# Kernel optimization log

Measured on AMD Instinct MI355X. Metric: run time of the kernel, lower is better.

## Reference

```python
import jax, jax.numpy as jnp
import numpy as np

N_FM = 100000; N_TP = 4096; N_SM = 100000
IN_FM = 64; IN_SM = 32; IN_TP = 32; IN_GF = 64; HID = 128
E_QOQ = 1000000; E_BP = 1000000; E_CP = 500000; E_CD = 500000; E_RB = 1000000


def setup_inputs():
    key = jax.random.key(0)
    ks = jax.random.split(key, 32)
    rn = lambda k, s, sc=0.05: jax.random.normal(k, s, jnp.float32) * sc
    inp = {}
    inp['x_fm'] = jax.random.normal(ks[0], (N_FM, IN_FM), jnp.float32)
    inp['x_sm'] = jax.random.normal(ks[1], (N_SM, IN_SM), jnp.float32)
    inp['period_vol'] = jax.random.uniform(ks[2], (N_TP, 1), jnp.float32)
    inp['gf'] = jax.random.normal(ks[3], (1, IN_GF), jnp.float32)
    inp['pe_table'] = rn(ks[4], (N_TP, IN_TP), 1.0)  # period_emb weight
    inp['qoq_src'] = jax.random.randint(ks[5], (E_QOQ,), 0, N_FM)
    inp['qoq_dst'] = jax.random.randint(ks[6], (E_QOQ,), 0, N_FM)
    inp['bp_src'] = jax.random.randint(ks[7], (E_BP,), 0, N_FM)
    inp['bp_dst'] = jax.random.randint(ks[8], (E_BP,), 0, N_TP)
    inp['cp_src'] = jax.random.randint(ks[9], (E_CP,), 0, N_TP)
    inp['cp_dst'] = jax.random.randint(ks[10], (E_CP,), 0, N_FM)
    inp['cd_src'] = jax.random.randint(ks[11], (E_CD,), 0, N_TP)
    inp['cd_dst'] = jax.random.randint(ks[12], (E_CD,), 0, N_SM)
    inp['rb_src'] = jax.random.randint(ks[13], (E_RB,), 0, N_TP)
    inp['rb_dst'] = jax.random.randint(ks[14], (E_RB,), 0, N_FM)
    i = 15
    # per-relation SAGEConv params: W_l [in_src,H] + bias, W_r [in_dst,H] (root, no bias)
    for name, ins, ind in [('qoq', IN_FM, IN_FM), ('bp', IN_FM, IN_TP), ('cp', IN_TP, IN_FM), ('cd', IN_TP, IN_SM), ('rb', IN_TP, IN_FM)]:
        inp[name + '_Wl'] = rn(ks[i], (ins, HID)); inp[name + '_bl'] = jnp.zeros((HID,), jnp.float32)
        inp[name + '_Wr'] = rn(ks[i + 1], (ind, HID)); i += 2
    for t in ['fm', 'tp', 'sm']:
        inp['ln_' + t + '_g'] = jnp.ones((HID,), jnp.float32)
        inp['ln_' + t + '_b'] = jnp.zeros((HID,), jnp.float32)
    inp['head_W1'] = rn(ks[i], (HID * 3 + IN_GF, HID // 2)); inp['head_b1'] = jnp.zeros((HID // 2,), jnp.float32)
    inp['head_W2'] = rn(ks[i + 1], (HID // 2, 1)); inp['head_b2'] = jnp.zeros((1,), jnp.float32)
    return inp


def _seg_mean(feat, dst, n):
    s = jax.ops.segment_sum(feat, dst, num_segments=n)
    c = jax.ops.segment_sum(jnp.ones((dst.shape[0], 1), feat.dtype), dst, num_segments=n)
    return s / jnp.maximum(c, 1.0)


def _sage(x_src, x_dst, src, dst, Wl, bl, Wr):
    # PyG SAGEConv: lin_l(mean_j x_j) + lin_r(x_i); aggregate raw features, then transform
    m = _seg_mean(x_src[src], dst, x_dst.shape[0])
    return m @ Wl + bl + x_dst @ Wr


def _ln(x, g, b, eps=1e-5):
    mu = x.mean(-1, keepdims=True)
    xc = x - mu
    var = (xc * xc).mean(-1, keepdims=True)
    return xc / jnp.sqrt(var + eps) * g + b


def _forward(x_fm, x_sm, period_vol, gf, pe_table,
             qoq_Wl, qoq_bl, qoq_Wr, bp_Wl, bp_bl, bp_Wr, cp_Wl, cp_bl, cp_Wr,
             cd_Wl, cd_bl, cd_Wr, rb_Wl, rb_bl, rb_Wr,
             ln_fm_g, ln_fm_b, ln_tp_g, ln_tp_b, ln_sm_g, ln_sm_b,
             head_W1, head_b1, head_W2, head_b2,
             qoq_src, qoq_dst, bp_src, bp_dst, cp_src, cp_dst, cd_src, cd_dst, rb_src, rb_dst):
    pe = pe_table * period_vol  # [T, in_tp]
    # HeteroConv aggr='mean': average relation outputs per destination type
    out_fm = (_sage(x_fm, x_fm, qoq_src, qoq_dst, qoq_Wl, qoq_bl, qoq_Wr)
              + _sage(pe, x_fm, cp_src, cp_dst, cp_Wl, cp_bl, cp_Wr)
              + _sage(pe, x_fm, rb_src, rb_dst, rb_Wl, rb_bl, rb_Wr)) / 3.0
    out_tp = _sage(x_fm, pe, bp_src, bp_dst, bp_Wl, bp_bl, bp_Wr)
    out_sm = _sage(pe, x_sm, cd_src, cd_dst, cd_Wl, cd_bl, cd_Wr)
    fm = jax.nn.relu(_ln(out_fm, ln_fm_g, ln_fm_b))
    tp = jax.nn.relu(_ln(out_tp, ln_tp_g, ln_tp_b))
    sm = jax.nn.relu(_ln(out_sm, ln_sm_g, ln_sm_b))
    h = jnp.concatenate([fm.mean(0), tp.mean(0), sm.mean(0), gf[0]], axis=-1)
    h = jax.nn.relu(h @ head_W1 + head_b1)  # dropout is identity in eval
    return (h @ head_W2 + head_b2).squeeze()


def reference(x_fm, x_sm, period_vol, gf, pe_table,
              qoq_src, qoq_dst, bp_src, bp_dst, cp_src, cp_dst, cd_src, cd_dst, rb_src, rb_dst,
              qoq_Wl, qoq_bl, qoq_Wr, bp_Wl, bp_bl, bp_Wr, cp_Wl, cp_bl, cp_Wr,
              cd_Wl, cd_bl, cd_Wr, rb_Wl, rb_bl, rb_Wr,
              ln_fm_g, ln_fm_b, ln_tp_g, ln_tp_b, ln_sm_g, ln_sm_b,
              head_W1, head_b1, head_W2, head_b2):
    return _forward(x_fm, x_sm, period_vol, gf, pe_table,
                    qoq_Wl, qoq_bl, qoq_Wr, bp_Wl, bp_bl, bp_Wr, cp_Wl, cp_bl, cp_Wr,
                    cd_Wl, cd_bl, cd_Wr, rb_Wl, rb_bl, rb_Wr,
                    ln_fm_g, ln_fm_b, ln_tp_g, ln_tp_b, ln_sm_g, ln_sm_b,
                    head_W1, head_b1, head_W2, head_b2,
                    qoq_src, qoq_dst, bp_src, bp_dst, cp_src, cp_dst, cd_src, cd_dst, rb_src, rb_dst)
```

## Files before the change

### kernel.cpp

```cpp
#include <hip/hip_runtime.h>
#include <hip/hip_fp16.h>

#define N_FM 100000
#define N_TP 4096
#define N_SM 100000
#define HID 128
#define E_QOQ 1000000
#define E_BP 1000000
#define E_CP 500000
#define E_CD 500000
#define E_RB 1000000
#define E_TOT 4000000

#define EO_CP  1000000
#define EO_RB  1500000
#define EO_BP  2500000
#define EO_CD  3500000

#define EL_QOQ 0
#define EL_CP  (N_FM)
#define EL_RB  (2 * N_FM)
#define EL_BP  (3 * N_FM)
#define EL_CD  (3 * N_FM + N_TP)
#define NTOT   (3 * N_FM + N_TP + N_SM)

#define BB_QOQ 0
#define BB_CP  782
#define BB_RB  1173
#define BB_BP  1564
#define BB_CD  1692
#define NBUCK  2083
#define CHUNK  4096
#define NCHUNK ((E_TOT + CHUNK - 1) / CHUNK)
#define EPB    (CHUNK / 256)

#define PAIRS_CAP 5784064

#define GRID_FM 768
#define GRID_TP 64
#define GRID_SM 1024

__device__ __forceinline__ int bucket_base(int b) {
    if (b < BB_CP) return b * 2048;
    if (b < BB_RB) return 1601536 + (b - BB_CP) * 2048;
    if (b < BB_BP) return 2402304 + (b - BB_RB) * 3584;
    if (b < BB_CD) return 3803648 + (b - BB_BP) * 9216;
    return 4983296 + (b - BB_CD) * 2048;
}

typedef _Float16 h2 __attribute__((ext_vector_type(2)));
typedef _Float16 f16x8_t __attribute__((ext_vector_type(8)));
typedef float f32x4_t __attribute__((ext_vector_type(4)));

union U32H2 { unsigned u; h2 h; };
union U4H8 { uint4 u; f16x8_t h; };

#if defined(__has_builtin)
#if __has_builtin(__builtin_amdgcn_fdot2)
#define HAVE_FDOT2 1
#endif
#endif

__device__ __forceinline__ unsigned pk2(float a, float b) {
    U32H2 x; x.h = h2{(_Float16)a, (_Float16)b}; return x.u;
}
__device__ __forceinline__ f16x8_t as_h8(uint4 v) { U4H8 x; x.u = v; return x.h; }

__device__ __forceinline__ float dot2sel(float acc, h2 v, h2 sel) {
#ifdef HAVE_FDOT2
    return __builtin_amdgcn_fdot2(v, sel, acc, false);
#else
    return acc + (float)v[0] * (float)sel[0] + (float)v[1] * (float)sel[1];
#endif
}

#define R1 (N_FM * 32)
#define R2 (R1 + N_SM * 16)
#define R3 (R2 + N_TP * 16)
#define R4 (R3 + 12288)
#define R5 (R4 + 6144)
#define R6 (R5 + 4096)
#define R7 (R6 + 128)

__device__ __forceinline__ unsigned pack_pair(const float* W, int p, int c) {
    return pk2(W[(2 * p) * HID + c], W[(2 * p + 1) * HID + c]);
}

__global__ void pack_all(const float* __restrict__ x_fm, const float* __restrict__ x_sm,
                         const float* __restrict__ pe_table, const float* __restrict__ pvol,
                         const float* __restrict__ qoq_Wl, const float* __restrict__ cp_Wl,
                         const float* __restrict__ rb_Wl, const float* __restrict__ qoq_Wr,
                         const float* __restrict__ cp_Wr, const float* __restrict__ rb_Wr,
                         const float* __restrict__ bp_Wl, const float* __restrict__ bp_Wr,
                         const float* __restrict__ cd_Wl, const float* __restrict__ cd_Wr,
                         const float* __restrict__ qoq_bl, const float* __restrict__ cp_bl,
                         const float* __restrict__ rb_bl,
                         unsigned* __restrict__ x_fm_f, unsigned* __restrict__ x_sm_f,
                         unsigned* __restrict__ pe_f, unsigned* __restrict__ wf_fm,
                         unsigned* __restrict__ wf_tp, unsigned* __restrict__ wf_sm,
                         float* __restrict__ bias_fm) {
    int gid = blockIdx.x * blockDim.x + threadIdx.x;
    if (gid < R1) {
        float2 t = ((const float2*)x_fm)[gid];
        x_fm_f[gid] = pk2(t.x, t.y);
    } else if (gid < R2) {
        int i = gid - R1;
        float2 t = ((const float2*)x_sm)[i];
        x_sm_f[i] = pk2(t.x, t.y);
    } else if (gid < R3) {
        int i = gid - R2;
        float2 t = ((const float2*)pe_table)[i];
        float v = pvol[i >> 4];
        pe_f[i] = pk2(t.x * v, t.y * v);
    } else if (gid < R4) {
        int j = gid - R3;
        int f = j >> 8, lr = (j >> 2) & 63, jj = j & 3;
        int p = (f >> 3) * 16 + ((lr >> 4) << 2) + jj;
        int c = (f & 7) * 16 + (lr & 15);
        unsigned v;
        if (p < 32) v = pack_pair(qoq_Wl, p, c);
        else if (p < 48) v = pack_pair(cp_Wl, p - 32, c);
        else if (p < 64) v = pack_pair(rb_Wl, p - 48, c);
        else {
            int pp = p - 64;
            float u0 = qoq_Wr[(2 * pp) * HID + c] + cp_Wr[(2 * pp) * HID + c] + rb_Wr[(2 * pp) * HID + c];
            float u1 = qoq_Wr[(2 * pp + 1) * HID + c] + cp_Wr[(2 * pp + 1) * HID + c] + rb_Wr[(2 * pp + 1) * HID + c];
            v = pk2(u0, u1);
        }
        wf_fm[j] = v;
    } else if (gid < R5) {
        int j = gid - R4;
        int f = j >> 8, lr = (j >> 2) & 63, jj = j & 3;
        int p = (f >> 3) * 16 + ((lr >> 4) << 2) + jj;
        int c = (f & 7) * 16 + (lr & 15);
        wf_tp[j] = (p < 32) ? pack_pair(bp_Wl, p, c) : pack_pair(bp_Wr, p - 32, c);
    } else if (gid < R6) {
        int j = gid - R5;
        int f = j >> 8, lr = (j >> 2) & 63, jj = j & 3;
        int p = (f >> 3) * 16 + ((lr >> 4) << 2) + jj;
        int c = (f & 7) * 16 + (lr & 15);
        wf_sm[j] = (p < 16) ? pack_pair(cd_Wl, p, c) : pack_pair(cd_Wr, p - 16, c);
    } else if (gid < R7) {
        int c = gid - R6;
        bias_fm[c] = qoq_bl[c] + cp_bl[c] + rb_bl[c];
    }
}

struct EdgePtrs {
    const int *qs, *qd, *cs, *cd_, *rs, *rd, *bs, *bd, *ds, *dd;
};

template <bool NEED_SRC>
__device__ __forceinline__ void edge_decode(const EdgePtrs& P, int e, int& bucket, int& dl, int& src) {
    const int* dp = P.qd; const int* sp = P.qs;
    int i = e, bb = BB_QOQ, sh = 7;
    if (e >= EO_CP) { i = e - EO_CP; dp = P.cd_; sp = P.cs; bb = BB_CP; sh = 8; }
    if (e >= EO_RB) { i = e - EO_RB; dp = P.rd;  sp = P.rs; bb = BB_RB; sh = 8; }
    if (e >= EO_BP) { i = e - EO_BP; dp = P.bd;  sp = P.bs; bb = BB_BP; sh = 5; }
    if (e >= EO_CD) { i = e - EO_CD; dp = P.dd;  sp = P.ds; bb = BB_CD; sh = 8; }
    int d = dp[i];
    bucket = bb + (d >> sh);
    dl = d & ((1 << sh) - 1);
    if (NEED_SRC) src = sp[i];
}

__global__ void __launch_bounds__(256) bin_kernel(EdgePtrs P, int* __restrict__ bwork,
                                                  unsigned* __restrict__ pairs) {
    __shared__ int lh[NBUCK];
    const int tid = threadIdx.x;
    for (int i = tid; i < NBUCK; i += 256) lh[i] = 0;
    __syncthreads();
    const int base = blockIdx.x * CHUNK;
    const int lim = min(base + CHUNK, E_TOT);
    unsigned ebd[EPB]; int esr[EPB];
#pragma unroll
    for (int j = 0; j < EPB; j++) {
        int e = base + tid + j * 256;
        if (e < lim) {
            int b, dl, s;
            edge_decode<true>(P, e, b, dl, s);
            ebd[j] = ((unsigned)b << 8) | (unsigned)dl;
            esr[j] = s;
            atomicAdd(&lh[b], 1);
        }
    }
    __syncthreads();
#pragma unroll
    for (int u = 0; u < (NBUCK + 255) / 256; u++) {
        int b = tid + u * 256;
        if (b < NBUCK) {
            int c = lh[b];
            lh[b] = c ? bucket_base(b) + atomicAdd(&bwork[b], c) : 0;
        }
    }
    __syncthreads();
#pragma unroll
    for (int j = 0; j < EPB; j++) {
        int e = base + tid + j * 256;
        if (e < lim) {
            int b = (int)(ebd[j] >> 8);
            int pos = atomicAdd(&lh[b], 1);
            pairs[pos] = ((ebd[j] & 255u) << 24) | (unsigned)esr[j];
        }
    }
}

__global__ void __launch_bounds__(256) esort(const int* __restrict__ bwork,
                                             const unsigned* __restrict__ pairs,
                                             int* __restrict__ so,
                                             int* __restrict__ el_beg, int* __restrict__ el_end) {
    __shared__ int hist[256], scn[256];
    __shared__ int so_lds[9216];
    const int b = blockIdx.x;
    const int tid = threadIdx.x;
    int beg = bucket_base(b);
    int end = beg + bwork[b];
    int egbase, ne;
    if (b < BB_CP)      { int e0 = (b - BB_QOQ) << 7; egbase = EL_QOQ + e0; ne = min(128, N_FM - e0); }
    else if (b < BB_RB) { int e0 = (b - BB_CP) << 8;  egbase = EL_CP + e0;  ne = min(256, N_FM - e0); }
    else if (b < BB_BP) { int e0 = (b - BB_RB) << 8;  egbase = EL_RB + e0;  ne = min(256, N_FM - e0); }
    else if (b < BB_CD) { int e0 = (b - BB_BP) << 5;  egbase = EL_BP + e0;  ne = min(32, N_TP - e0); }
    else                { int e0 = (b - BB_CD) << 8;  egbase = EL_CD + e0;  ne = min(256, N_SM - e0); }
    hist[tid] = 0;
    __syncthreads();
    for (int e = beg + tid; e < end; e += 256)
        atomicAdd(&hist[pairs[e] >> 24], 1);
    __syncthreads();
    int v = hist[tid];
    scn[tid] = v;
    __syncthreads();
    for (int off = 1; off < 256; off <<= 1) {
        int u = (tid >= off) ? scn[tid - off] : 0;
        __syncthreads();
        scn[tid] += u;
        __syncthreads();
    }
    int excl = scn[tid] - v;
    if (tid < ne) {
        el_beg[egbase + tid] = beg + excl;
        el_end[egbase + tid] = beg + excl + v;
    }
    hist[tid] = excl;
    __syncthreads();
    for (int e = beg + tid; e < end; e += 256) {
        unsigned pr = pairs[e];
        int dl = pr >> 24;
        int pos = atomicAdd(&hist[dl], 1);
        so_lds[pos] = (int)(pr & 0xFFFFFF);
    }
    __syncthreads();
    const int n = end - beg;
    for (int i = tid; i < n; i += 256) so[beg + i] = so_lds[i];
}

template <int LOGP, int NPRO>
__device__ __forceinline__ void gather_one(int g, int lane, const int* __restrict__ begs,
                                           const int* __restrict__ ends,
                                           const int* __restrict__ ssrc,
                                           const unsigned* __restrict__ feat,
                                           unsigned* __restrict__ mean) {
    const int P = 1 << LOGP;
    const h2 SLO = h2{(_Float16)1.0f, (_Float16)0.0f};
    const h2 SHI = h2{(_Float16)0.0f, (_Float16)1.0f};
    int beg = begs[g], end = ends[g];
    int n = end - beg;
    float alo = 0.0f, ahi = 0.0f;
    if (n > 0) {
        const int nm1 = n - 1;
        int s[NPRO];
#pragma unroll
        for (int j = 0; j < NPRO; j++) s[j] = ssrc[beg + min(j, nm1)];
        unsigned v[NPRO];
#pragma unroll
        for (int j = 0; j < NPRO; j++) v[j] = feat[(size_t)(unsigned)s[j] * P + lane];
#pragma unroll
        for (int j = 0; j < NPRO; j++) {
            U32H2 u; u.u = (j < n) ? v[j] : 0u;
            alo = dot2sel(alo, u.h, SLO); ahi = dot2sel(ahi, u.h, SHI);
        }
        int i = beg + NPRO;
        for (; i + 8 <= end; i += 8) {
            int t0 = ssrc[i],     t1 = ssrc[i + 1], t2 = ssrc[i + 2], t3 = ssrc[i + 3];
            int t4 = ssrc[i + 4], t5 = ssrc[i + 5], t6 = ssrc[i + 6], t7 = ssrc[i + 7];
            unsigned w0 = feat[(size_t)t0 * P + lane];
            unsigned w1 = feat[(size_t)t1 * P + lane];
            unsigned w2 = feat[(size_t)t2 * P + lane];
            unsigned w3 = feat[(size_t)t3 * P + lane];
            unsigned w4 = feat[(size_t)t4 * P + lane];
            unsigned w5 = feat[(size_t)t5 * P + lane];
            unsigned w6 = feat[(size_t)t6 * P + lane];
            unsigned w7 = feat[(size_t)t7 * P + lane];
            U32H2 u;
            u.u = w0; alo = dot2sel(alo, u.h, SLO); ahi = dot2sel(ahi, u.h, SHI);
            u.u = w1; alo = dot2sel(alo, u.h, SLO); ahi = dot2sel(ahi, u.h, SHI);
            u.u = w2; alo = dot2sel(alo, u.h, SLO); ahi = dot2sel(ahi, u.h, SHI);
            u.u = w3; alo = dot2sel(alo, u.h, SLO); ahi = dot2sel(ahi, u.h, SHI);
            u.u = w4; alo = dot2sel(alo, u.h, SLO); ahi = dot2sel(ahi, u.h, SHI);
            u.u = w5; alo = dot2sel(alo, u.h, SLO); ahi = dot2sel(ahi, u.h, SHI);
            u.u = w6; alo = dot2sel(alo, u.h, SLO); ahi = dot2sel(ahi, u.h, SHI);
            u.u = w7; alo = dot2sel(alo, u.h, SLO); ahi = dot2sel(ahi, u.h, SHI);
        }
        for (; i < end; i++) {
            U32H2 u; u.u = feat[(size_t)ssrc[i] * P + lane];
            alo = dot2sel(alo, u.h, SLO); ahi = dot2sel(ahi, u.h, SHI);
        }
    }
    float ic = (n > 0) ? 1.0f / (float)n : 0.0f;
    mean[(size_t)g * P + lane] = pk2(alo * ic, ahi * ic);
}

#define G1 (N_TP * 32)
#define G2 (G1 + N_FM * 32)
#define G3 (G2 + N_FM * 16)
#define G4 (G3 + N_SM * 16)
#define G5 (G4 + N_FM * 16)

__global__ void __launch_bounds__(256)
gather_all(const int* __restrict__ el_beg, const int* __restrict__ el_end,
           const int* __restrict__ so_all,
           const unsigned* __restrict__ x_fm_f, const unsigned* __restrict__ pe_f,
           unsigned* __restrict__ mean_qoq, unsigned* __restrict__ mean_cp,
           unsigned* __restrict__ mean_rb, unsigned* __restrict__ mean_bp,
           unsigned* __restrict__ mean_cd) {
    int gid = blockIdx.x * blockDim.x + threadIdx.x;
    if (gid < G1) {
        gather_one<5, 16>(gid >> 5, gid & 31, el_beg + EL_BP, el_end + EL_BP, so_all, x_fm_f, mean_bp);
    } else if (gid < G2) {
        int i = gid - G1;
        gather_one<5, 16>(i >> 5, i & 31, el_beg + EL_QOQ, el_end + EL_QOQ, so_all, x_fm_f, mean_qoq);
    } else if (gid < G3) {
        int i = gid - G2;
        gather_one<4, 8>(i >> 4, i & 15, el_beg + EL_CP, el_end + EL_CP, so_all, pe_f, mean_cp);
    } else if (gid < G4) {
        int i = gid - G3;
        gather_one<4, 8>(i >> 4, i & 15, el_beg + EL_CD, el_end + EL_CD, so_all, pe_f, mean_cd);
    } else if (gid < G5) {
        int i = gid - G4;
        gather_one<4, 16>(i >> 4, i & 15, el_beg + EL_RB, el_end + EL_RB, so_all, pe_f, mean_rb);
    }
}


__global__ void __launch_bounds__(256)
fm_mfma(const unsigned* __restrict__ mq, const unsigned* __restrict__ mc,
        const unsigned* __restrict__ mr, const unsigned* __restrict__ xf,
        const unsigned* __restrict__ wfrag, const float* __restrict__ bias,
        const float* __restrict__ ln_g, const float* __restrict__ ln_b,
        float* __restrict__ part) {
    __shared__ uint4 wlds[48 * 64];
    const int tid = threadIdx.x, lane = tid & 63, wid = tid >> 6;
    for (int i = tid; i < 48 * 64; i += 256) wlds[i] = ((const uint4*)wfrag)[i];
    const int c0 = lane & 15, ko = lane >> 4;
    float bias_[8], g_[8], b_[8], colacc[8];
#pragma unroll
    for (int nt = 0; nt < 8; nt++) {
        int c = nt * 16 + c0;
        bias_[nt] = bias[c]; g_[nt] = ln_g[c]; b_[nt] = ln_b[c]; colacc[nt] = 0.0f;
    }
    __syncthreads();
    const f32x4_t zero = {0.0f, 0.0f, 0.0f, 0.0f};
    const int ntiles = N_FM / 16;
    for (int tile = blockIdx.x * 4 + wid; tile < ntiles; tile += gridDim.x * 4) {
        const size_t row = (size_t)tile * 16 + c0;
        uint4 av[6];
        av[0] = ((const uint4*)mq)[row * 8 + ko];
        av[1] = ((const uint4*)mq)[row * 8 + 4 + ko];
        av[2] = ((const uint4*)mc)[row * 4 + ko];
        av[3] = ((const uint4*)mr)[row * 4 + ko];
        av[4] = ((const uint4*)xf)[row * 8 + ko];
        av[5] = ((const uint4*)xf)[row * 8 + 4 + ko];
        f32x4_t acc[8];
#pragma unroll
        for (int nt = 0; nt < 8; nt++) acc[nt] = zero;
#pragma unroll
        for (int ks = 0; ks < 6; ks++) {
            f16x8_t af = as_h8(av[ks]);
#pragma unroll
            for (int nt = 0; nt < 8; nt++)
                acc[nt] = __builtin_amdgcn_mfma_f32_16x16x32_f16(
                    af, as_h8(wlds[(ks * 8 + nt) * 64 + lane]), acc[nt], 0, 0, 0);
        }
#pragma unroll
        for (int r = 0; r < 4; r++) {
            float yv[8]; float s = 0.0f, q = 0.0f;
#pragma unroll
            for (int nt = 0; nt < 8; nt++) {
                float y = (acc[nt][r] + bias_[nt]) * (1.0f / 3.0f);
                yv[nt] = y; s += y; q += y * y;
            }
#pragma unroll
            for (int off = 1; off < 16; off <<= 1) { s += __shfl_xor(s, off); q += __shfl_xor(q, off); }
            float mu = s * (1.0f / 128.0f);
            float var = fmaxf(q * (1.0f / 128.0f) - mu * mu, 0.0f);
            float rs = rsqrtf(var + 1e-5f);
#pragma unroll
            for (int nt = 0; nt < 8; nt++)
                colacc[nt] += fmaxf((yv[nt] - mu) * rs * g_[nt] + b_[nt], 0.0f);
        }
    }
#pragma unroll
    for (int nt = 0; nt < 8; nt++) {
        colacc[nt] += __shfl_xor(colacc[nt], 16);
        colacc[nt] += __shfl_xor(colacc[nt], 32);
    }
    __syncthreads();
    float* sred = (float*)wlds;
    if (lane < 16) {
#pragma unroll
        for (int nt = 0; nt < 8; nt++) sred[wid * 128 + nt * 16 + lane] = colacc[nt];
    }
    __syncthreads();
    if (tid < 128)
        part[(size_t)blockIdx.x * 128 + tid] =
            sred[tid] + sred[128 + tid] + sred[256 + tid] + sred[384 + tid];
}

template <int KSA, int KSB>
__global__ void __launch_bounds__(256)
rows_mfma(int ntiles, const unsigned* __restrict__ mA, const unsigned* __restrict__ xB,
          const unsigned* __restrict__ wfrag, const float* __restrict__ bl,
          const float* __restrict__ ln_g, const float* __restrict__ ln_b,
          float* __restrict__ part) {
    constexpr int KS = KSA + KSB;
    __shared__ uint4 wlds[KS * 8 * 64];
    const int tid = threadIdx.x, lane = tid & 63, wid = tid >> 6;
    for (int i = tid; i < KS * 8 * 64; i += 256) wlds[i] = ((const uint4*)wfrag)[i];
    const int c0 = lane & 15, ko = lane >> 4;
    float bias_[8], g_[8], b_[8], colacc[8];
#pragma unroll
    for (int nt = 0; nt < 8; nt++) {
        int c = nt * 16 + c0;
        bias_[nt] = bl[c]; g_[nt] = ln_g[c]; b_[nt] = ln_b[c]; colacc[nt] = 0.0f;
    }
    __syncthreads();
    const f32x4_t zero = {0.0f, 0.0f, 0.0f, 0.0f};
    for (int tile = blockIdx.x * 4 + wid; tile < ntiles; tile += gridDim.x * 4) {
        const size_t row = (size_t)tile * 16 + c0;
        uint4 av[KS];
#pragma unroll
        for (int ks = 0; ks < KSA; ks++) av[ks] = ((const uint4*)mA)[row * (KSA * 4) + ks * 4 + ko];
#pragma unroll
        for (int ks = 0; ks < KSB; ks++) av[KSA + ks] = ((const uint4*)xB)[row * (KSB * 4) + ks * 4 + ko];
        f32x4_t acc[8];
#pragma unroll
        for (int nt = 0; nt < 8; nt++) acc[nt] = zero;
#pragma unroll
        for (int ks = 0; ks < KS; ks++) {
            f16x8_t af = as_h8(av[ks]);
#pragma unroll
            for (int nt = 0; nt < 8; nt++)
                acc[nt] = __builtin_amdgcn_mfma_f32_16x16x32_f16(
                    af, as_h8(wlds[(ks * 8 + nt) * 64 + lane]), acc[nt], 0, 0, 0);
        }
#pragma unroll
        for (int r = 0; r < 4; r++) {
            float yv[8]; float s = 0.0f, q = 0.0f;
#pragma unroll
            for (int nt = 0; nt < 8; nt++) {
                float y = acc[nt][r] + bias_[nt];
                yv[nt] = y; s += y; q += y * y;
            }
#pragma unroll
            for (int off = 1; off < 16; off <<= 1) { s += __shfl_xor(s, off); q += __shfl_xor(q, off); }
            float mu = s * (1.0f / 128.0f);
            float var = fmaxf(q * (1.0f / 128.0f) - mu * mu, 0.0f);
            float rs = rsqrtf(var + 1e-5f);
#pragma unroll
            for (int nt = 0; nt < 8; nt++)
                colacc[nt] += fmaxf((yv[nt] - mu) * rs * g_[nt] + b_[nt], 0.0f);
        }
    }
#pragma unroll
    for (int nt = 0; nt < 8; nt++) {
        colacc[nt] += __shfl_xor(colacc[nt], 16);
        colacc[nt] += __shfl_xor(colacc[nt], 32);
    }
    __syncthreads();
    float* sred = (float*)wlds;
    if (lane < 16) {
#pragma unroll
        for (int nt = 0; nt < 8; nt++) sred[wid * 128 + nt * 16 + lane] = colacc[nt];
    }
    __syncthreads();
    if (tid < 128)
        part[(size_t)blockIdx.x * 128 + tid] =
            sred[tid] + sred[128 + tid] + sred[256 + tid] + sred[384 + tid];
}

__global__ void __launch_bounds__(512)
reduce_cols(const float* __restrict__ part, float* __restrict__ colsum) {
    __shared__ float lds[512];
    const int t = threadIdx.x, col = t & 127, sl = t >> 7;
    int cnt, srcoff, dst;
    if (blockIdx.x == 0)      { cnt = GRID_FM; srcoff = 0;                         dst = 0;   }
    else if (blockIdx.x == 1) { cnt = GRID_TP; srcoff = GRID_FM * 128;             dst = 128; }
    else                      { cnt = GRID_SM; srcoff = (GRID_FM + GRID_TP) * 128; dst = 256; }
    float a = 0.0f;
    for (int i = sl; i < cnt; i += 4) a += part[srcoff + i * 128 + col];
    lds[t] = a;
    __syncthreads();
    if (t < 128) colsum[dst + t] = lds[t] + lds[128 + t] + lds[256 + t] + lds[384 + t];
}

__global__ void head_kernel(const float* __restrict__ colsum, const float* __restrict__ gf,
                            const float* __restrict__ W1, const float* __restrict__ b1,
                            const float* __restrict__ W2, const float* __restrict__ b2,
                            float* __restrict__ out) {
    __shared__ float h[448];
    __shared__ float sh[512];
    __shared__ float h1[64];
    int t = threadIdx.x;
    if (t < 128) h[t] = colsum[t] * (1.0f / N_FM);
    else if (t < 256) h[t] = colsum[t] * (1.0f / N_TP);
    else if (t < 384) h[t] = colsum[t] * (1.0f / N_SM);
    else if (t < 448) h[t] = gf[t - 384];
    __syncthreads();
    {
        int col = t & 63, slice = t >> 6;
        float a = 0.0f;
        for (int k = slice * 56; k < slice * 56 + 56; k++) a += h[k] * W1[k * 64 + col];
        sh[slice * 64 + col] = a;
    }
    __syncthreads();
    if (t < 64) {
        float a = b1[t];
#pragma unroll
        for (int s = 0; s < 8; s++) a += sh[s * 64 + t];
        h1[t] = fmaxf(a, 0.0f);
    }
    __syncthreads();
    if (t < 64) {
        float p = h1[t] * W2[t];
#pragma unroll
        for (int off = 1; off < 64; off <<= 1) p += __shfl_xor(p, off);
        if (t == 0) out[0] = p + b2[0];
    }
}

extern "C" void kernel_launch(void* const* d_in, const int* in_sizes, int n_in,
                              void* d_out, int out_size, void* d_ws, size_t ws_size,
                              hipStream_t stream) {
    const float* x_fm = (const float*)d_in[0];
    const float* x_sm = (const float*)d_in[1];
    const float* period_vol = (const float*)d_in[2];
    const float* gf = (const float*)d_in[3];
    const float* pe_table = (const float*)d_in[4];
    const int* qoq_src = (const int*)d_in[5];
    const int* qoq_dst = (const int*)d_in[6];
    const int* bp_src = (const int*)d_in[7];
    const int* bp_dst = (const int*)d_in[8];
    const int* cp_src = (const int*)d_in[9];
    const int* cp_dst = (const int*)d_in[10];
    const int* cd_src = (const int*)d_in[11];
    const int* cd_dst = (const int*)d_in[12];
    const int* rb_src = (const int*)d_in[13];
    const int* rb_dst = (const int*)d_in[14];
    const float* qoq_Wl = (const float*)d_in[15];
    const float* qoq_bl = (const float*)d_in[16];
    const float* qoq_Wr = (const float*)d_in[17];
    const float* bp_Wl = (const float*)d_in[18];
    const float* bp_bl = (const float*)d_in[19];
    const float* bp_Wr = (const float*)d_in[20];
    const float* cp_Wl = (const float*)d_in[21];
    const float* cp_bl = (const float*)d_in[22];
    const float* cp_Wr = (const float*)d_in[23];
    const float* cd_Wl = (const float*)d_in[24];
    const float* cd_bl = (const float*)d_in[25];
    const float* cd_Wr = (const float*)d_in[26];
    const float* rb_Wl = (const float*)d_in[27];
    const float* rb_bl = (const float*)d_in[28];
    const float* rb_Wr = (const float*)d_in[29];
    const float* ln_fm_g = (const float*)d_in[30];
    const float* ln_fm_b = (const float*)d_in[31];
    const float* ln_tp_g = (const float*)d_in[32];
    const float* ln_tp_b = (const float*)d_in[33];
    const float* ln_sm_g = (const float*)d_in[34];
    const float* ln_sm_b = (const float*)d_in[35];
    const float* head_W1 = (const float*)d_in[36];
    const float* head_b1 = (const float*)d_in[37];
    const float* head_W2 = (const float*)d_in[38];
    const float* head_b2 = (const float*)d_in[39];

    unsigned* wsu = (unsigned*)d_ws;
    size_t off = 0;
    int* bwork = (int*)(wsu + off); off += NBUCK;
    float* colsum = (float*)(wsu + off); off += 384;
    size_t zero_words = off;
    off = (off + 3) & ~(size_t)3;
    unsigned* pairs = wsu + off; off += PAIRS_CAP;
    int* so_all = (int*)(wsu + off); off += PAIRS_CAP;
    int* el_beg = (int*)(wsu + off); off += NTOT;
    int* el_end = (int*)(wsu + off); off += NTOT;
    unsigned* mean_qoq = wsu + off; off += (size_t)N_FM * 32;
    unsigned* mean_cp  = wsu + off; off += (size_t)N_FM * 16;
    unsigned* mean_rb  = wsu + off; off += (size_t)N_FM * 16;
    unsigned* mean_bp  = wsu + off; off += (size_t)N_TP * 32;
    unsigned* mean_cd  = wsu + off; off += (size_t)N_SM * 16;
    unsigned* pe_f     = wsu + off; off += (size_t)N_TP * 16;
    unsigned* x_fm_f   = wsu + off; off += (size_t)N_FM * 32;
    unsigned* x_sm_f   = wsu + off; off += (size_t)N_SM * 16;
    unsigned* wf_fm    = wsu + off; off += 12288;
    unsigned* wf_tp    = wsu + off; off += 6144;
    unsigned* wf_sm    = wsu + off; off += 4096;
    float* bias_fm     = (float*)(wsu + off); off += 128;

    float* part_fm = (float*)pairs;
    float* part_tp = part_fm + GRID_FM * 128;
    float* part_sm = part_tp + GRID_TP * 128;

    hipMemsetAsync(d_ws, 0, zero_words * 4, stream);

    pack_all<<<(R7 + 255) / 256, 256, 0, stream>>>(
        x_fm, x_sm, pe_table, period_vol, qoq_Wl, cp_Wl, rb_Wl, qoq_Wr, cp_Wr, rb_Wr,
        bp_Wl, bp_Wr, cd_Wl, cd_Wr, qoq_bl, cp_bl, rb_bl,
        x_fm_f, x_sm_f, pe_f, wf_fm, wf_tp, wf_sm, bias_fm);

    EdgePtrs EP{qoq_src, qoq_dst, cp_src, cp_dst, rb_src, rb_dst, bp_src, bp_dst, cd_src, cd_dst};

    bin_kernel<<<NCHUNK, 256, 0, stream>>>(EP, bwork, pairs);
    esort<<<NBUCK, 256, 0, stream>>>(bwork, pairs, so_all, el_beg, el_end);
    gather_all<<<(G5 + 255) / 256, 256, 0, stream>>>(el_beg, el_end, so_all, x_fm_f, pe_f,
                                                     mean_qoq, mean_cp, mean_rb, mean_bp, mean_cd);

    fm_mfma<<<GRID_FM, 256, 0, stream>>>(mean_qoq, mean_cp, mean_rb, x_fm_f, wf_fm,
                                         bias_fm, ln_fm_g, ln_fm_b, part_fm);
    rows_mfma<2, 1><<<GRID_TP, 256, 0, stream>>>(N_TP / 16, mean_bp, pe_f, wf_tp,
                                                 bp_bl, ln_tp_g, ln_tp_b, part_tp);
    rows_mfma<1, 1><<<GRID_SM, 256, 0, stream>>>(N_SM / 16, mean_cd, x_sm_f, wf_sm,
                                                 cd_bl, ln_sm_g, ln_sm_b, part_sm);

    reduce_cols<<<3, 512, 0, stream>>>(part_fm, colsum);

    head_kernel<<<1, 512, 0, stream>>>(colsum, gf, head_W1, head_b1, head_W2, head_b2,
                                       (float*)d_out);
}
```

Before: 432.9 us.

## Replace bucket binning and local sort with global count, scan, scatter CSR build

Edges are now grouped by destination with per-node global atomic counts, a three-kernel prefix scan and an atomic scatter of sources, replacing the two-level bucket-bin plus per-bucket LDS counting sort. This drops the intermediate pairs buffer and its capacity layout, but puts one global atomic per edge in two passes and adds three extra launches. The pack kernel also moves to float4 loads with two packed half2 outputs per thread. Source order within a destination is no longer deterministic, which may change fp16 summation order slightly.

```diff
diff --git a/kernel.cpp b/kernel.cpp
--- a/kernel.cpp
+++ b/kernel.cpp
@@ -24,29 +24,16 @@
 #define EL_CD  (3 * N_FM + N_TP)
 #define NTOT   (3 * N_FM + N_TP + N_SM)
 
-#define BB_QOQ 0
-#define BB_CP  782
-#define BB_RB  1173
-#define BB_BP  1564
-#define BB_CD  1692
-#define NBUCK  2083
 #define CHUNK  4096
 #define NCHUNK ((E_TOT + CHUNK - 1) / CHUNK)
 #define EPB    (CHUNK / 256)
 
-#define PAIRS_CAP 5784064
+#define ELPB   2048
+#define SBLK   ((NTOT + ELPB - 1) / ELPB)
 
 #define GRID_FM 768
 #define GRID_TP 64
 #define GRID_SM 1024
-
-__device__ __forceinline__ int bucket_base(int b) {
-    if (b < BB_CP) return b * 2048;
-    if (b < BB_RB) return 1601536 + (b - BB_CP) * 2048;
-    if (b < BB_BP) return 2402304 + (b - BB_RB) * 3584;
-    if (b < BB_CD) return 3803648 + (b - BB_BP) * 9216;
-    return 4983296 + (b - BB_CD) * 2048;
-}
 
 typedef _Float16 h2 __attribute__((ext_vector_type(2)));
 typedef _Float16 f16x8_t __attribute__((ext_vector_type(8)));
@@ -74,9 +61,9 @@
 #endif
 }
 
-#define R1 (N_FM * 32)
-#define R2 (R1 + N_SM * 16)
-#define R3 (R2 + N_TP * 16)
+#define R1 (N_FM * 16)
+#define R2 (R1 + N_SM * 8)
+#define R3 (R2 + N_TP * 8)
 #define R4 (R3 + 12288)
 #define R5 (R4 + 6144)
 #define R6 (R5 + 4096)
@@ -101,17 +88,20 @@
                          float* __restrict__ bias_fm) {
     int gid = blockIdx.x * blockDim.x + threadIdx.x;
     if (gid < R1) {
-        float2 t = ((const float2*)x_fm)[gid];
-        x_fm_f[gid] = pk2(t.x, t.y);
+        float4 t = ((const float4*)x_fm)[gid];
+        uint2 o; o.x = pk2(t.x, t.y); o.y = pk2(t.z, t.w);
+        ((uint2*)x_fm_f)[gid] = o;
     } else if (gid < R2) {
         int i = gid - R1;
-        float2 t = ((const float2*)x_sm)[i];
-        x_sm_f[i] = pk2(t.x, t.y);
+        float4 t = ((const float4*)x_sm)[i];
+        uint2 o; o.x = pk2(t.x, t.y); o.y = pk2(t.z, t.w);
+        ((uint2*)x_sm_f)[i] = o;
     } else if (gid < R3) {
         int i = gid - R2;
-        float2 t = ((const float2*)pe_table)[i];
-        float v = pvol[i >> 4];
-        pe_f[i] = pk2(t.x * v, t.y * v);
+        float4 t = ((const float4*)pe_table)[i];
+        float v = pvol[i >> 3];
+        uint2 o; o.x = pk2(t.x * v, t.y * v); o.y = pk2(t.z * v, t.w * v);
+        ((uint2*)pe_f)[i] = o;
     } else if (gid < R4) {
         int j = gid - R3;
         int f = j >> 8, lr = (j >> 2) & 63, jj = j & 3;
@@ -151,119 +141,138 @@
 };
 
 template <bool NEED_SRC>
-__device__ __forceinline__ void edge_decode(const EdgePtrs& P, int e, int& bucket, int& dl, int& src) {
+__device__ __forceinline__ void edge_elem(const EdgePtrs& P, int e, int& elem, int& src) {
     const int* dp = P.qd; const int* sp = P.qs;
-    int i = e, bb = BB_QOQ, sh = 7;
-    if (e >= EO_CP) { i = e - EO_CP; dp = P.cd_; sp = P.cs; bb = BB_CP; sh = 8; }
-    if (e >= EO_RB) { i = e - EO_RB; dp = P.rd;  sp = P.rs; bb = BB_RB; sh = 8; }
-    if (e >= EO_BP) { i = e - EO_BP; dp = P.bd;  sp = P.bs; bb = BB_BP; sh = 5; }
-    if (e >= EO_CD) { i = e - EO_CD; dp = P.dd;  sp = P.ds; bb = BB_CD; sh = 8; }
-    int d = dp[i];
-    bucket = bb + (d >> sh);
-    dl = d & ((1 << sh) - 1);
+    int i = e, eb = EL_QOQ;
+    if (e >= EO_CP) { i = e - EO_CP; dp = P.cd_; sp = P.cs; eb = EL_CP; }
+    if (e >= EO_RB) { i = e - EO_RB; dp = P.rd;  sp = P.rs; eb = EL_RB; }
+    if (e >= EO_BP) { i = e - EO_BP; dp = P.bd;  sp = P.bs; eb = EL_BP; }
+    if (e >= EO_CD) { i = e - EO_CD; dp = P.dd;  sp = P.ds; eb = EL_CD; }
+    elem = eb + dp[i];
     if (NEED_SRC) src = sp[i];
 }
 
-__global__ void __launch_bounds__(256) bin_kernel(EdgePtrs P, int* __restrict__ bwork,
-                                                  unsigned* __restrict__ pairs) {
-    __shared__ int lh[NBUCK];
+__global__ void __launch_bounds__(256) count_kernel(EdgePtrs P, int* __restrict__ el_cnt) {
     const int tid = threadIdx.x;
-    for (int i = tid; i < NBUCK; i += 256) lh[i] = 0;
-    __syncthreads();
     const int base = blockIdx.x * CHUNK;
     const int lim = min(base + CHUNK, E_TOT);
-    unsigned ebd[EPB]; int esr[EPB];
-#pragma unroll
-    for (int j = 0; j < EPB; j++) {
-        int e = base + tid + j * 256;
-        if (e < lim) {
-            int b, dl, s;
-            edge_decode<true>(P, e, b, dl, s);
-            ebd[j] = ((unsigned)b << 8) | (unsigned)dl;
-            esr[j] = s;
-            atomicAdd(&lh[b], 1);
-        }
-    }
-    __syncthreads();
-#pragma unroll
-    for (int u = 0; u < (NBUCK + 255) / 256; u++) {
-        int b = tid + u * 256;
-        if (b < NBUCK) {
-            int c = lh[b];
-            lh[b] = c ? bucket_base(b) + atomicAdd(&bwork[b], c) : 0;
-        }
-    }
-    __syncthreads();
-#pragma unroll
-    for (int j = 0; j < EPB; j++) {
-        int e = base + tid + j * 256;
-        if (e < lim) {
-            int b = (int)(ebd[j] >> 8);
-            int pos = atomicAdd(&lh[b], 1);
-            pairs[pos] = ((ebd[j] & 255u) << 24) | (unsigned)esr[j];
-        }
-    }
-}
-
-__global__ void __launch_bounds__(256) esort(const int* __restrict__ bwork,
-                                             const unsigned* __restrict__ pairs,
-                                             int* __restrict__ so,
-                                             int* __restrict__ el_beg, int* __restrict__ el_end) {
-    __shared__ int hist[256], scn[256];
-    __shared__ int so_lds[9216];
-    const int b = blockIdx.x;
+#pragma unroll
+    for (int jj = 0; jj < EPB; jj += 4) {
+        int el[4];
+#pragma unroll
+        for (int k = 0; k < 4; k++) {
+            int e = base + tid + (jj + k) * 256;
+            int s;
+            if (e < lim) edge_elem<false>(P, e, el[k], s);
+            else el[k] = -1;
+        }
+#pragma unroll
+        for (int k = 0; k < 4; k++)
+            if (el[k] >= 0) atomicAdd(&el_cnt[el[k]], 1);
+    }
+}
+
+__global__ void __launch_bounds__(256) scan_local(const int* __restrict__ cnt,
+                                                  int* __restrict__ lofs,
+                                                  int* __restrict__ bsums) {
+    __shared__ int ts[256];
     const int tid = threadIdx.x;
-    int beg = bucket_base(b);
-    int end = beg + bwork[b];
-    int egbase, ne;
-    if (b < BB_CP)      { int e0 = (b - BB_QOQ) << 7; egbase = EL_QOQ + e0; ne = min(128, N_FM - e0); }
-    else if (b < BB_RB) { int e0 = (b - BB_CP) << 8;  egbase = EL_CP + e0;  ne = min(256, N_FM - e0); }
-    else if (b < BB_BP) { int e0 = (b - BB_RB) << 8;  egbase = EL_RB + e0;  ne = min(256, N_FM - e0); }
-    else if (b < BB_CD) { int e0 = (b - BB_BP) << 5;  egbase = EL_BP + e0;  ne = min(32, N_TP - e0); }
-    else                { int e0 = (b - BB_CD) << 8;  egbase = EL_CD + e0;  ne = min(256, N_SM - e0); }
-    hist[tid] = 0;
-    __syncthreads();
-    for (int e = beg + tid; e < end; e += 256)
-        atomicAdd(&hist[pairs[e] >> 24], 1);
-    __syncthreads();
-    int v = hist[tid];
-    scn[tid] = v;
+    const int base = blockIdx.x * ELPB + tid * 8;
+    int v[8]; int s = 0;
+#pragma unroll
+    for (int j = 0; j < 8; j++) {
+        int id = base + j;
+        v[j] = (id < NTOT) ? cnt[id] : 0;
+        s += v[j];
+    }
+    ts[tid] = s;
     __syncthreads();
     for (int off = 1; off < 256; off <<= 1) {
-        int u = (tid >= off) ? scn[tid - off] : 0;
+        int u = (tid >= off) ? ts[tid - off] : 0;
         __syncthreads();
-        scn[tid] += u;
+        ts[tid] += u;
         __syncthreads();
     }
-    int excl = scn[tid] - v;
-    if (tid < ne) {
-        el_beg[egbase + tid] = beg + excl;
-        el_end[egbase + tid] = beg + excl + v;
-    }
-    hist[tid] = excl;
-    __syncthreads();
-    for (int e = beg + tid; e < end; e += 256) {
-        unsigned pr = pairs[e];
-        int dl = pr >> 24;
-        int pos = atomicAdd(&hist[dl], 1);
-        so_lds[pos] = (int)(pr & 0xFFFFFF);
-    }
-    __syncthreads();
-    const int n = end - beg;
-    for (int i = tid; i < n; i += 256) so[beg + i] = so_lds[i];
+    int run = ts[tid] - s;
+#pragma unroll
+    for (int j = 0; j < 8; j++) {
+        int id = base + j;
+        if (id < NTOT) lofs[id] = run;
+        run += v[j];
+    }
+    if (tid == 255) bsums[blockIdx.x] = ts[255];
+}
+
+__global__ void __launch_bounds__(256) scan_tops(const int* __restrict__ bsums,
+                                                 int* __restrict__ boffs) {
+    __shared__ int ts[256];
+    const int tid = threadIdx.x;
+    int v = (tid < SBLK) ? bsums[tid] : 0;
+    ts[tid] = v;
+    __syncthreads();
+    for (int off = 1; off < 256; off <<= 1) {
+        int u = (tid >= off) ? ts[tid - off] : 0;
+        __syncthreads();
+        ts[tid] += u;
+        __syncthreads();
+    }
+    if (tid < SBLK) boffs[tid] = ts[tid] - v;
+}
+
+__global__ void __launch_bounds__(256) scan_apply(const int* __restrict__ lofs,
+                                                  const int* __restrict__ boffs,
+                                                  int* __restrict__ el_beg,
+                                                  int* __restrict__ el_cur) {
+    const int tid = threadIdx.x;
+    const int base = blockIdx.x * ELPB + tid * 8;
+    const int b = boffs[blockIdx.x];
+#pragma unroll
+    for (int j = 0; j < 8; j++) {
+        int id = base + j;
+        if (id < NTOT) {
+            int v = lofs[id] + b;
+            el_beg[id] = v;
+            el_cur[id] = v;
+        }
+    }
+}
+
+__global__ void __launch_bounds__(256) scatter_kernel(EdgePtrs P, int* __restrict__ el_cur,
+                                                      int* __restrict__ so) {
+    const int tid = threadIdx.x;
+    const int base = blockIdx.x * CHUNK;
+    const int lim = min(base + CHUNK, E_TOT);
+#pragma unroll
+    for (int jj = 0; jj < EPB; jj += 4) {
+        int el[4], sr[4];
+#pragma unroll
+        for (int k = 0; k < 4; k++) {
+            int e = base + tid + (jj + k) * 256;
+            if (e < lim) edge_elem<true>(P, e, el[k], sr[k]);
+            else el[k] = -1;
+        }
+        int pos[4];
+#pragma unroll
+        for (int k = 0; k < 4; k++)
+            pos[k] = (el[k] >= 0) ? atomicAdd(&el_cur[el[k]], 1) : 0;
+#pragma unroll
+        for (int k = 0; k < 4; k++)
+            if (el[k] >= 0) so[pos[k]] = sr[k];
+    }
 }
 
 template <int LOGP, int NPRO>
 __device__ __forceinline__ void gather_one(int g, int lane, const int* __restrict__ begs,
-                                           const int* __restrict__ ends,
+                                           const int* __restrict__ cnts,
                                            const int* __restrict__ ssrc,
                                            const unsigned* __restrict__ feat,
                                            unsigned* __restrict__ mean) {
     const int P = 1 << LOGP;
     const h2 SLO = h2{(_Float16)1.0f, (_Float16)0.0f};
     const h2 SHI = h2{(_Float16)0.0f, (_Float16)1.0f};
-    int beg = begs[g], end = ends[g];
-    int n = end - beg;
+    int beg = begs[g];
+    int n = cnts[g];
+    int end = beg + n;
     float alo = 0.0f, ahi = 0.0f;
     if (n > 0) {
         const int nm1 = n - 1;
@@ -316,7 +325,7 @@
 #define G5 (G4 + N_FM * 16)
 
 __global__ void __launch_bounds__(256)
-gather_all(const int* __restrict__ el_beg, const int* __restrict__ el_end,
+gather_all(const int* __restrict__ el_beg, const int* __restrict__ el_cnt,
            const int* __restrict__ so_all,
            const unsigned* __restrict__ x_fm_f, const unsigned* __restrict__ pe_f,
            unsigned* __restrict__ mean_qoq, unsigned* __restrict__ mean_cp,
@@ -324,19 +333,19 @@
            unsigned* __restrict__ mean_cd) {
     int gid = blockIdx.x * blockDim.x + threadIdx.x;
     if (gid < G1) {
-        gather_one<5, 16>(gid >> 5, gid & 31, el_beg + EL_BP, el_end + EL_BP, so_all, x_fm_f, mean_bp);
+        gather_one<5, 16>(gid >> 5, gid & 31, el_beg + EL_BP, el_cnt + EL_BP, so_all, x_fm_f, mean_bp);
     } else if (gid < G2) {
         int i = gid - G1;
-        gather_one<5, 16>(i >> 5, i & 31, el_beg + EL_QOQ, el_end + EL_QOQ, so_all, x_fm_f, mean_qoq);
+        gather_one<5, 16>(i >> 5, i & 31, el_beg + EL_QOQ, el_cnt + EL_QOQ, so_all, x_fm_f, mean_qoq);
     } else if (gid < G3) {
         int i = gid - G2;
-        gather_one<4, 8>(i >> 4, i & 15, el_beg + EL_CP, el_end + EL_CP, so_all, pe_f, mean_cp);
+        gather_one<4, 8>(i >> 4, i & 15, el_beg + EL_CP, el_cnt + EL_CP, so_all, pe_f, mean_cp);
     } else if (gid < G4) {
         int i = gid - G3;
-        gather_one<4, 8>(i >> 4, i & 15, el_beg + EL_CD, el_end + EL_CD, so_all, pe_f, mean_cd);
+        gather_one<4, 8>(i >> 4, i & 15, el_beg + EL_CD, el_cnt + EL_CD, so_all, pe_f, mean_cd);
     } else if (gid < G5) {
         int i = gid - G4;
-        gather_one<4, 16>(i >> 4, i & 15, el_beg + EL_RB, el_end + EL_RB, so_all, pe_f, mean_rb);
+        gather_one<4, 16>(i >> 4, i & 15, el_beg + EL_RB, el_cnt + EL_RB, so_all, pe_f, mean_rb);
     }
 }
 
@@ -583,14 +592,16 @@
 
     unsigned* wsu = (unsigned*)d_ws;
     size_t off = 0;
-    int* bwork = (int*)(wsu + off); off += NBUCK;
     float* colsum = (float*)(wsu + off); off += 384;
+    int* el_cnt = (int*)(wsu + off); off += NTOT;
     size_t zero_words = off;
     off = (off + 3) & ~(size_t)3;
-    unsigned* pairs = wsu + off; off += PAIRS_CAP;
-    int* so_all = (int*)(wsu + off); off += PAIRS_CAP;
+    int* so_all = (int*)(wsu + off); off += E_TOT;
     int* el_beg = (int*)(wsu + off); off += NTOT;
-    int* el_end = (int*)(wsu + off); off += NTOT;
+    int* el_cur = (int*)(wsu + off); off += NTOT;
+    int* lofs   = (int*)(wsu + off); off += NTOT;
+    int* bsums  = (int*)(wsu + off); off += 256;
+    int* boffs  = (int*)(wsu + off); off += 256;
     unsigned* mean_qoq = wsu + off; off += (size_t)N_FM * 32;
     unsigned* mean_cp  = wsu + off; off += (size_t)N_FM * 16;
     unsigned* mean_rb  = wsu + off; off += (size_t)N_FM * 16;
@@ -604,7 +615,7 @@
     unsigned* wf_sm    = wsu + off; off += 4096;
     float* bias_fm     = (float*)(wsu + off); off += 128;
 
-    float* part_fm = (float*)pairs;
+    float* part_fm = (float*)so_all;
     float* part_tp = part_fm + GRID_FM * 128;
     float* part_sm = part_tp + GRID_TP * 128;
 
@@ -617,9 +628,13 @@
 
     EdgePtrs EP{qoq_src, qoq_dst, cp_src, cp_dst, rb_src, rb_dst, bp_src, bp_dst, cd_src, cd_dst};
 
-    bin_kernel<<<NCHUNK, 256, 0, stream>>>(EP, bwork, pairs);
-    esort<<<NBUCK, 256, 0, stream>>>(bwork, pairs, so_all, el_beg, el_end);
-    gather_all<<<(G5 + 255) / 256, 256, 0, stream>>>(el_beg, el_end, so_all, x_fm_f, pe_f,
+    count_kernel<<<NCHUNK, 256, 0, stream>>>(EP, el_cnt);
+    scan_local<<<SBLK, 256, 0, stream>>>(el_cnt, lofs, bsums);
+    scan_tops<<<1, 256, 0, stream>>>(bsums, boffs);
+    scan_apply<<<SBLK, 256, 0, stream>>>(lofs, boffs, el_beg, el_cur);
+    scatter_kernel<<<NCHUNK, 256, 0, stream>>>(EP, el_cur, so_all);
+
+    gather_all<<<(G5 + 255) / 256, 256, 0, stream>>>(el_beg, el_cnt, so_all, x_fm_f, pe_f,
                                                      mean_qoq, mean_cp, mean_rb, mean_bp, mean_cd);
 
     fm_mfma<<<GRID_FM, 256, 0, stream>>>(mean_qoq, mean_cp, mean_rb, x_fm_f, wf_fm,
```

Result: slower. 816.5 us (+88.6%).
